# Performance work log

Hardware: AMD Instinct MI355X
Metric: run time of the kernel (lower is better)

Reference implementation:

```python
import jax, jax.numpy as jnp
import numpy as np
from jax.scipy.special import logsumexp

N_STATES = 64
N_OBS = 10000
BATCH = 256
T_MAX = 2048


def setup_inputs() -> dict:
    key = jax.random.key(0)
    k1, k2, k3, k4, k5 = jax.random.split(key, 5)
    x = jax.random.randint(k1, (BATCH, T_MAX), 0, N_OBS, dtype=jnp.int64 if jax.config.jax_enable_x64 else jnp.int32)
    T = jax.random.randint(k2, (BATCH,), 1, T_MAX + 1, dtype=x.dtype)  # lengths in [1, T_MAX]
    pi = jnp.zeros((N_STATES,), dtype=jnp.float32)
    unnormalized_transition_matrix = jax.random.normal(k3, (N_STATES, N_STATES), dtype=jnp.float32)
    unnormalized_emission_matrix = jax.random.normal(k4, (N_STATES, N_OBS), dtype=jnp.float32)
    return {
        "x": x,
        "T": T,
        "pi": pi,
        "unnormalized_transition_matrix": unnormalized_transition_matrix,
        "unnormalized_emission_matrix": unnormalized_emission_matrix,
    }


def reference(x, T, pi, unnormalized_transition_matrix, unnormalized_emission_matrix):
    # log p(x) via the log-domain forward algorithm.
    log_pi = jax.nn.log_softmax(pi, axis=0)                                  # [N]
    log_A = jax.nn.log_softmax(unnormalized_transition_matrix, axis=0)       # [N, N], A[i,k] = p(i | k)-style per torch dim=0
    log_E = jax.nn.log_softmax(unnormalized_emission_matrix, axis=1)         # [N, M]

    # emissions[b, t, n] = log_E[n, x[b, t]]  (gather once, not per step)
    emis = log_E.T[x]                                                        # [B, Tm, N]

    alpha0 = emis[:, 0, :] + log_pi                                          # [B, N]

    def step(alpha, e_t):
        # new_alpha[b, i] = e_t[b, i] + logsumexp_k (log_A[i, k] + alpha[b, k])
        new = e_t + logsumexp(log_A[None, :, :] + alpha[:, None, :], axis=2)
        return new, new

    _, alphas = jax.lax.scan(step, alpha0, jnp.swapaxes(emis[:, 1:, :], 0, 1))  # [Tm-1, B, N]
    log_alpha = jnp.concatenate([alpha0[None], alphas], axis=0)              # [Tm, B, N]

    log_sums = logsumexp(log_alpha, axis=2).T                                # [B, Tm]
    idx = (T - 1).astype(jnp.int32)[:, None]
    log_probs = jnp.take_along_axis(log_sums, idx, axis=1)                   # [B, 1]
    return log_probs
```

## Files before the change

### kernel.cpp

```cpp
#include <hip/hip_runtime.h>
#include <math.h>

#define NS   64
#define NOBS 10000
#define NB   256
#define TMAX 2048

#define PIP_OFF 0
#define ASW_OFF 64
#define LSE_OFF (64 + 4096)
#define ET_OFF  (64 + 4096 + 64)

__device__ __forceinline__ float wsum64(float v) {
  v += __shfl_xor(v, 1);
  v += __shfl_xor(v, 2);
  v += __shfl_xor(v, 4);
  v += __shfl_xor(v, 8);
  v += __shfl_xor(v, 16);
  v += __shfl_xor(v, 32);
  return v;
}

#define DPPROR(S, N)                                                           \
  __int_as_float(__builtin_amdgcn_update_dpp(                                  \
      0, __float_as_int(S), 0x120 + (N), 0xF, 0xF, true))

#define COMB(Q) ({                                                             \
    float a32_ = (Q); float b32_;                                              \
    asm("v_mov_b32 %0, %1" : "=v"(b32_) : "v"(a32_));                          \
    asm("v_permlane32_swap_b32 %0, %1" : "+v"(a32_), "+v"(b32_));              \
    float s32_ = a32_ + b32_;                                                  \
    float a16_ = s32_; float b16_;                                             \
    asm("v_mov_b32 %0, %1" : "=v"(b16_) : "v"(s32_));                          \
    asm("v_permlane16_swap_b32 %0, %1" : "+v"(a16_), "+v"(b16_));              \
    a16_ + b16_; })

__global__ __launch_bounds__(64) void prep_small(const float* __restrict__ pi,
                                                 const float* __restrict__ A,
                                                 float* __restrict__ ws) {
  const int l = threadIdx.x;
  const int r = l & 15, c = l >> 4;
  float p = pi[l];
  float m = p;
  m = fmaxf(m, __shfl_xor(m, 1));
  m = fmaxf(m, __shfl_xor(m, 2));
  m = fmaxf(m, __shfl_xor(m, 4));
  m = fmaxf(m, __shfl_xor(m, 8));
  m = fmaxf(m, __shfl_xor(m, 16));
  m = fmaxf(m, __shfl_xor(m, 32));
  float ex = expf(p - m);
  float s = wsum64(ex);
  ws[PIP_OFF + l] = ex / s;

  __shared__ float Ap[NS * NS];
  float cm = -3.0e38f;
  for (int i = 0; i < NS; ++i) cm = fmaxf(cm, A[i * NS + l]);
  float cs = 0.f;
  for (int i = 0; i < NS; ++i) cs += expf(A[i * NS + l] - cm);
  float inv = 1.0f / cs;
  for (int i = 0; i < NS; ++i) Ap[i * NS + l] = expf(A[i * NS + l] - cm) * inv;
  __syncthreads();

  const int probe = __builtin_amdgcn_update_dpp(0, l, 0x121, 0xF, 0xF, true);
  const int dir = ((probe & 15) == ((r - 1) & 15)) ? 1 : -1;

  for (int g = 0; g < 4; ++g)
    for (int j = 0; j < 16; ++j)
      ws[ASW_OFF + l * 64 + g * 16 + j] =
          Ap[(r + 16 * g) * NS + (16 * c + ((r - dir * j) & 15))];
}

__global__ __launch_bounds__(256) void emis_lse(const float* __restrict__ E,
                                                float* __restrict__ ws) {
  const int s = blockIdx.x;
  const float* row = E + (size_t)s * NOBS;
  __shared__ float red[4];
  float m = -3.0e38f;
  for (int o = threadIdx.x; o < NOBS; o += 256) m = fmaxf(m, row[o]);
  m = fmaxf(m, __shfl_xor(m, 1));
  m = fmaxf(m, __shfl_xor(m, 2));
  m = fmaxf(m, __shfl_xor(m, 4));
  m = fmaxf(m, __shfl_xor(m, 8));
  m = fmaxf(m, __shfl_xor(m, 16));
  m = fmaxf(m, __shfl_xor(m, 32));
  const int wid = threadIdx.x >> 6;
  if ((threadIdx.x & 63) == 0) red[wid] = m;
  __syncthreads();
  m = fmaxf(fmaxf(red[0], red[1]), fmaxf(red[2], red[3]));
  __syncthreads();
  float sum = 0.f;
  for (int o = threadIdx.x; o < NOBS; o += 256) sum += expf(row[o] - m);
  sum = wsum64(sum);
  if ((threadIdx.x & 63) == 0) red[wid] = sum;
  __syncthreads();
  if (threadIdx.x == 0)
    ws[LSE_OFF + s] = m + logf(red[0] + red[1] + red[2] + red[3]);
}

__global__ __launch_bounds__(256) void emis_fill(const float* __restrict__ E,
                                                 float* __restrict__ ws) {
  const int idx = blockIdx.x * 256 + threadIdx.x;
  if (idx >= NS * NOBS) return;
  const int s = idx & 63;
  const int obs = idx >> 6;
  ws[ET_OFF + idx] = expf(E[(size_t)s * NOBS + obs] - ws[LSE_OFF + s]);
}


#define PIN8(i)                                                                \
  asm volatile("" : "+v"(aw[(i)]), "+v"(aw[(i) + 1]), "+v"(aw[(i) + 2]),       \
                    "+v"(aw[(i) + 3]), "+v"(aw[(i) + 4]), "+v"(aw[(i) + 5]),   \
                    "+v"(aw[(i) + 6]), "+v"(aw[(i) + 7]))
#define PIN_AW() do { PIN8(0); PIN8(8); PIN8(16); PIN8(24);                    \
                      PIN8(32); PIN8(40); PIN8(48); PIN8(56); } while (0)

#define STAGE_CHUNK(XS, HALF) do {                                             \
    _Pragma("unroll")                                                          \
    for (int k_ = 0; k_ < 64; ++k_) {                                          \
      const int xt_ = __builtin_amdgcn_readlane((XS), k_);                     \
      const float* gp_ = ET + ((size_t)(unsigned)xt_ << 6) + lane;             \
      __builtin_amdgcn_global_load_lds(gp_, &ebuf[(((HALF) << 6) + k_) << 6],  \
                                       4, 0, 0);                               \
    } } while (0)

#define EREAD(DST, ADDR, IMM)                                                  \
  asm volatile("ds_read_b32 %0, %1 offset:" #IMM : "=v"(DST) : "v"(ADDR))

#define STEP(u, EC) do {                                                       \
    const int t_ = t0 + (u);                                                   \
    const float e_ = EC[(u)];                                                  \
    const unsigned srf_ = __builtin_amdgcn_readfirstlane(__float_as_uint(s));  \
    const int se_ = (int)((srf_ >> 23) & 0xFFu) - 127;                         \
    const float sc_ = __uint_as_float((unsigned)(127 - se_) << 23);            \
    const float es_ = e_ * sc_;                                                \
    float rot[16];                                                             \
    rot[0] = s;                                                                \
    rot[1] = DPPROR(s, 1);   rot[2] = DPPROR(s, 2);   rot[3] = DPPROR(s, 3);   \
    rot[4] = DPPROR(s, 4);   rot[5] = DPPROR(s, 5);   rot[6] = DPPROR(s, 6);   \
    rot[7] = DPPROR(s, 7);   rot[8] = DPPROR(s, 8);   rot[9] = DPPROR(s, 9);   \
    rot[10] = DPPROR(s, 10); rot[11] = DPPROR(s, 11); rot[12] = DPPROR(s, 12); \
    rot[13] = DPPROR(s, 13); rot[14] = DPPROR(s, 14); rot[15] = DPPROR(s, 15); \
    float q0a_ = 0.f, q1a_ = 0.f, q2a_ = 0.f, q3a_ = 0.f;                      \
    float q0b_ = 0.f, q1b_ = 0.f, q2b_ = 0.f, q3b_ = 0.f;                      \
    _Pragma("unroll")                                                          \
    for (int j_ = 0; j_ < 8; ++j_) {                                           \
      q0a_ = fmaf(aw[j_],      rot[j_], q0a_);                                 \
      q1a_ = fmaf(aw[16 + j_], rot[j_], q1a_);                                 \
      q2a_ = fmaf(aw[32 + j_], rot[j_], q2a_);                                 \
      q3a_ = fmaf(aw[48 + j_], rot[j_], q3a_);                                 \
      q0b_ = fmaf(aw[8 + j_],  rot[8 + j_], q0b_);                             \
      q1b_ = fmaf(aw[24 + j_], rot[8 + j_], q1b_);                             \
      q2b_ = fmaf(aw[40 + j_], rot[8 + j_], q2b_);                             \
      q3b_ = fmaf(aw[56 + j_], rot[8 + j_], q3b_);                             \
    }                                                                          \
    const float tot0_ = COMB(q0a_ + q0b_);                                     \
    const float tot1_ = COMB(q1a_ + q1b_);                                     \
    const float tot2_ = COMB(q2a_ + q2b_);                                     \
    const float tot3_ = COMB(q3a_ + q3b_);                                     \
    const float ta_ = (cgrp & 1) ? tot1_ : tot0_;                              \
    const float tb_ = (cgrp & 1) ? tot3_ : tot2_;                              \
    const float sel_ = (cgrp & 2) ? tb_ : ta_;                                 \
    const float w_ = es_ * ((t_ == 0) ? pip : sel_);                           \
    E2 += se_;                                                                 \
    if (t_ == Tn - 1) { vs = w_; e2s = E2; }                                   \
    s = w_;                                                                    \
  } while (0)

#define GROUP(T0, ECUR, ENXT) do {                                             \
    const int t0 = (T0);                                                       \
    { const unsigned ea_ =                                                     \
          ebase + ((unsigned)(((t0 + 4) & 127)) << 8) + ((unsigned)lane << 2); \
      EREAD(ENXT[0], ea_, 0);   EREAD(ENXT[1], ea_, 256);                      \
      EREAD(ENXT[2], ea_, 512); EREAD(ENXT[3], ea_, 768); }                    \
    asm volatile("s_waitcnt lgkmcnt(4)");                                      \
    __builtin_amdgcn_sched_barrier(0);                                         \
    STEP(0, ECUR); STEP(1, ECUR); STEP(2, ECUR); STEP(3, ECUR);                \
  } while (0)

__global__ void __attribute__((amdgpu_flat_work_group_size(64, 64)))
__attribute__((amdgpu_waves_per_eu(1, 1)))
hmm_fwd(const int* __restrict__ x, const int* __restrict__ T,
        const float* __restrict__ ws, float* __restrict__ out) {
  const int lane = threadIdx.x;
  const int b = blockIdx.x;
  const int cgrp = lane >> 4;
  const float* __restrict__ ET = ws + ET_OFF;
  const int* __restrict__ xb = x + (size_t)b * TMAX;
  const int Tn = T[b];

  __shared__ __align__(16) float ebuf[128 * 64];
  const unsigned ebase = (unsigned)(size_t)ebuf;

  float aw[NS];
  {
    const float4* ar = (const float4*)(ws + ASW_OFF + lane * NS);
#pragma unroll
    for (int q = 0; q < 16; ++q) {
      float4 f = ar[q];
      aw[4 * q + 0] = f.x; aw[4 * q + 1] = f.y;
      aw[4 * q + 2] = f.z; aw[4 * q + 3] = f.w;
    }
  }
  PIN_AW();

  const float pip = ws[PIP_OFF + lane];

  int xcur = xb[lane];
  STAGE_CHUNK(xcur, 0);
  int xnext = xb[64 + lane];
  asm volatile("s_waitcnt vmcnt(0)" ::: "memory");

  float eA[4], eB[4];
  {
    const unsigned ea_ = ebase + ((unsigned)lane << 2);
    EREAD(eA[0], ea_, 0);   EREAD(eA[1], ea_, 256);
    EREAD(eA[2], ea_, 512); EREAD(eA[3], ea_, 768);
  }

  float s = 1.0f;
  float vs = 0.f;
  int E2 = 0, e2s = 0;

  const int nch = (Tn + 63) >> 6;
  for (int c = 0; c < nch; ++c) {
    const int tb = c << 6;
    if (c + 1 < TMAX / 64) STAGE_CHUNK(xnext, (c + 1) & 1);
    xnext = ((c + 2) < TMAX / 64) ? xb[((c + 2) << 6) + lane] : 0;
#pragma unroll 1
    for (int gp = 0; gp < 7; ++gp) {
      GROUP(tb + (gp << 3), eA, eB);
      GROUP(tb + (gp << 3) + 4, eB, eA);
    }
    GROUP(tb + 56, eA, eB);
    asm volatile("s_waitcnt vmcnt(0)" ::: "memory");
    GROUP(tb + 60, eB, eA);
  }

  const float sf = wsum64(vs);
  if (lane == 0) {
    const double lp = (double)logf(sf) + (double)e2s * 0.6931471805599453;
    out[b] = (float)lp;
  }
}

extern "C" void kernel_launch(void* const* d_in, const int* in_sizes, int n_in,
                              void* d_out, int out_size, void* d_ws, size_t ws_size,
                              hipStream_t stream) {
  const int*   x  = (const int*)d_in[0];
  const int*   T  = (const int*)d_in[1];
  const float* pi = (const float*)d_in[2];
  const float* A  = (const float*)d_in[3];
  const float* E  = (const float*)d_in[4];
  float* out = (float*)d_out;
  float* ws  = (float*)d_ws;

  prep_small<<<1, 64, 0, stream>>>(pi, A, ws);
  emis_lse<<<NS, 256, 0, stream>>>(E, ws);
  emis_fill<<<(NS * NOBS + 255) / 256, 256, 0, stream>>>(E, ws);
  hmm_fwd<<<NB, 64, 0, stream>>>(x, T, ws, out);
}
```

Before: 462.2 us.

## Use packed FP32 FMA for the transition matvec and rescale every other step

Reorders the swizzled transition matrix so each lane holds pairs of rows (r, r+16) and (r+32, r+48) as float2. The per-step 64-term dot product then runs as v_pk_fma_f32 with the rotated state broadcast, halving the FMA instruction count on the serial critical path. Exponent rescaling via readfirstlane now happens only on odd steps, which removes scalar work but lets values grow over two steps before renormalising. This carries some overflow/underflow risk and relies on inline asm for the packed ops.

Result: slower. 483.2 us (+4.5%).

```diff
diff --git a/kernel.cpp b/kernel.cpp
--- a/kernel.cpp
+++ b/kernel.cpp
@@ -24,6 +24,15 @@
 #define DPPROR(S, N)                                                           \
   __int_as_float(__builtin_amdgcn_update_dpp(                                  \
       0, __float_as_int(S), 0x120 + (N), 0xF, 0xF, true))
+
+#define PKMUL(ACC, AP, RT)                                                     \
+  asm("v_pk_mul_f32 %0, %1, %2 op_sel:[0,0] op_sel_hi:[1,0]"                   \
+      : "=v"(ACC) : "v"(AP), "v"(RT))
+#define PKFMA(ACC, AP, RT)                                                     \
+  asm("v_pk_fma_f32 %0, %1, %2, %3 op_sel:[0,0,0] op_sel_hi:[1,0,1]"           \
+      : "=v"(ACC) : "v"(AP), "v"(RT), "v"(ACC))
+#define PKADD(D, X, Y)                                                         \
+  asm("v_pk_add_f32 %0, %1, %2" : "=v"(D) : "v"(X), "v"(Y))
 
 #define COMB(Q) ({                                                             \
     float a32_ = (Q); float b32_;                                              \
@@ -64,10 +73,13 @@
   const int probe = __builtin_amdgcn_update_dpp(0, l, 0x121, 0xF, 0xF, true);
   const int dir = ((probe & 15) == ((r - 1) & 15)) ? 1 : -1;
 
-  for (int g = 0; g < 4; ++g)
-    for (int j = 0; j < 16; ++j)
-      ws[ASW_OFF + l * 64 + g * 16 + j] =
-          Ap[(r + 16 * g) * NS + (16 * c + ((r - dir * j) & 15))];
+  for (int j = 0; j < 16; ++j) {
+    const int col = 16 * c + ((r - dir * j) & 15);
+    ws[ASW_OFF + l * 64 + 2 * j]          = Ap[(r + 0)  * NS + col];
+    ws[ASW_OFF + l * 64 + 2 * j + 1]      = Ap[(r + 16) * NS + col];
+    ws[ASW_OFF + l * 64 + 32 + 2 * j]     = Ap[(r + 32) * NS + col];
+    ws[ASW_OFF + l * 64 + 32 + 2 * j + 1] = Ap[(r + 48) * NS + col];
+  }
 }
 
 __global__ __launch_bounds__(256) void emis_lse(const float* __restrict__ E,
@@ -107,12 +119,11 @@
 }
 
 
-#define PIN8(i)                                                                \
-  asm volatile("" : "+v"(aw[(i)]), "+v"(aw[(i) + 1]), "+v"(aw[(i) + 2]),       \
-                    "+v"(aw[(i) + 3]), "+v"(aw[(i) + 4]), "+v"(aw[(i) + 5]),   \
-                    "+v"(aw[(i) + 6]), "+v"(aw[(i) + 7]))
-#define PIN_AW() do { PIN8(0); PIN8(8); PIN8(16); PIN8(24);                    \
-                      PIN8(32); PIN8(40); PIN8(48); PIN8(56); } while (0)
+#define PINP(P) asm volatile("" : "+v"((P).x), "+v"((P).y))
+#define PIN_ALL() do {                                                         \
+    _Pragma("unroll")                                                          \
+    for (int q_ = 0; q_ < 16; ++q_) { PINP(a01[q_]); PINP(a23[q_]); }          \
+  } while (0)
 
 #define STAGE_CHUNK(XS, HALF) do {                                             \
     _Pragma("unroll")                                                          \
@@ -129,39 +140,48 @@
 #define STEP(u, EC) do {                                                       \
     const int t_ = t0 + (u);                                                   \
     const float e_ = EC[(u)];                                                  \
-    const unsigned srf_ = __builtin_amdgcn_readfirstlane(__float_as_uint(s));  \
-    const int se_ = (int)((srf_ >> 23) & 0xFFu) - 127;                         \
-    const float sc_ = __uint_as_float((unsigned)(127 - se_) << 23);            \
-    const float es_ = e_ * sc_;                                                \
-    float rot[16];                                                             \
-    rot[0] = s;                                                                \
-    rot[1] = DPPROR(s, 1);   rot[2] = DPPROR(s, 2);   rot[3] = DPPROR(s, 3);   \
-    rot[4] = DPPROR(s, 4);   rot[5] = DPPROR(s, 5);   rot[6] = DPPROR(s, 6);   \
-    rot[7] = DPPROR(s, 7);   rot[8] = DPPROR(s, 8);   rot[9] = DPPROR(s, 9);   \
-    rot[10] = DPPROR(s, 10); rot[11] = DPPROR(s, 11); rot[12] = DPPROR(s, 12); \
-    rot[13] = DPPROR(s, 13); rot[14] = DPPROR(s, 14); rot[15] = DPPROR(s, 15); \
-    float q0a_ = 0.f, q1a_ = 0.f, q2a_ = 0.f, q3a_ = 0.f;                      \
-    float q0b_ = 0.f, q1b_ = 0.f, q2b_ = 0.f, q3b_ = 0.f;                      \
+    float es_;                                                                 \
+    if (((u) & 1) != 0) {               \
+      const unsigned srf_ = __builtin_amdgcn_readfirstlane(__float_as_uint(s));\
+      const int se_ = (int)((srf_ >> 23) & 0xFFu) - 127;                       \
+      const float sc_ = __uint_as_float((unsigned)(127 - se_) << 23);          \
+      es_ = e_ * sc_;                                                          \
+      E2 += se_;                                                               \
+    } else {                                                                   \
+      es_ = e_;                                                                \
+    }                                                                          \
+    rot2[0].x = s;                                                             \
+    rot2[1].x = DPPROR(s, 1);   rot2[2].x = DPPROR(s, 2);                      \
+    rot2[3].x = DPPROR(s, 3);   rot2[4].x = DPPROR(s, 4);                      \
+    rot2[5].x = DPPROR(s, 5);   rot2[6].x = DPPROR(s, 6);                      \
+    rot2[7].x = DPPROR(s, 7);   rot2[8].x = DPPROR(s, 8);                      \
+    rot2[9].x = DPPROR(s, 9);   rot2[10].x = DPPROR(s, 10);                    \
+    rot2[11].x = DPPROR(s, 11); rot2[12].x = DPPROR(s, 12);                    \
+    rot2[13].x = DPPROR(s, 13); rot2[14].x = DPPROR(s, 14);                    \
+    rot2[15].x = DPPROR(s, 15);                                                \
+    float2 ac01a, ac01b, ac23a, ac23b;                                         \
+    PKMUL(ac01a, a01[0], rot2[0]);                                             \
+    PKMUL(ac23a, a23[0], rot2[0]);                                             \
+    PKMUL(ac01b, a01[8], rot2[8]);                                             \
+    PKMUL(ac23b, a23[8], rot2[8]);                                             \
     _Pragma("unroll")                                                          \
-    for (int j_ = 0; j_ < 8; ++j_) {                                           \
-      q0a_ = fmaf(aw[j_],      rot[j_], q0a_);                                 \
-      q1a_ = fmaf(aw[16 + j_], rot[j_], q1a_);                                 \
-      q2a_ = fmaf(aw[32 + j_], rot[j_], q2a_);                                 \
-      q3a_ = fmaf(aw[48 + j_], rot[j_], q3a_);                                 \
-      q0b_ = fmaf(aw[8 + j_],  rot[8 + j_], q0b_);                             \
-      q1b_ = fmaf(aw[24 + j_], rot[8 + j_], q1b_);                             \
-      q2b_ = fmaf(aw[40 + j_], rot[8 + j_], q2b_);                             \
-      q3b_ = fmaf(aw[56 + j_], rot[8 + j_], q3b_);                             \
+    for (int j_ = 1; j_ < 8; ++j_) {                                           \
+      PKFMA(ac01a, a01[j_],     rot2[j_]);                                     \
+      PKFMA(ac23a, a23[j_],     rot2[j_]);                                     \
+      PKFMA(ac01b, a01[8 + j_], rot2[8 + j_]);                                 \
+      PKFMA(ac23b, a23[8 + j_], rot2[8 + j_]);                                 \
     }                                                                          \
-    const float tot0_ = COMB(q0a_ + q0b_);                                     \
-    const float tot1_ = COMB(q1a_ + q1b_);                                     \
-    const float tot2_ = COMB(q2a_ + q2b_);                                     \
-    const float tot3_ = COMB(q3a_ + q3b_);                                     \
+    float2 s01_, s23_;                                                         \
+    PKADD(s01_, ac01a, ac01b);                                                 \
+    PKADD(s23_, ac23a, ac23b);                                                 \
+    const float tot0_ = COMB(s01_.x);                                          \
+    const float tot1_ = COMB(s01_.y);                                          \
+    const float tot2_ = COMB(s23_.x);                                          \
+    const float tot3_ = COMB(s23_.y);                                          \
     const float ta_ = (cgrp & 1) ? tot1_ : tot0_;                              \
     const float tb_ = (cgrp & 1) ? tot3_ : tot2_;                              \
     const float sel_ = (cgrp & 2) ? tb_ : ta_;                                 \
     const float w_ = es_ * ((t_ == 0) ? pip : sel_);                           \
-    E2 += se_;                                                                 \
     if (t_ == Tn - 1) { vs = w_; e2s = E2; }                                   \
     s = w_;                                                                    \
   } while (0)
@@ -191,19 +211,29 @@
   __shared__ __align__(16) float ebuf[128 * 64];
   const unsigned ebase = (unsigned)(size_t)ebuf;
 
-  float aw[NS];
+  float2 a01[16], a23[16];
   {
     const float4* ar = (const float4*)(ws + ASW_OFF + lane * NS);
 #pragma unroll
-    for (int q = 0; q < 16; ++q) {
+    for (int q = 0; q < 8; ++q) {
       float4 f = ar[q];
-      aw[4 * q + 0] = f.x; aw[4 * q + 1] = f.y;
-      aw[4 * q + 2] = f.z; aw[4 * q + 3] = f.w;
+      a01[2 * q]     = make_float2(f.x, f.y);
+      a01[2 * q + 1] = make_float2(f.z, f.w);
     }
-  }
-  PIN_AW();
+#pragma unroll
+    for (int q = 0; q < 8; ++q) {
+      float4 f = ar[8 + q];
+      a23[2 * q]     = make_float2(f.x, f.y);
+      a23[2 * q + 1] = make_float2(f.z, f.w);
+    }
+  }
+  PIN_ALL();
 
   const float pip = ws[PIP_OFF + lane];
+
+  float2 rot2[16];
+#pragma unroll
+  for (int j = 0; j < 16; ++j) rot2[j].y = 0.0f;
 
   int xcur = xb[lane];
   STAGE_CHUNK(xcur, 0);
```

## Fuse DPP rotations into FMAs and use transpose-style cross-row reduction

Applied to the files above, without the earlier changes.

Replaces the separate DPP row-rotate moves plus FMAs with inline-asm v_fmac_f32_dpp instructions that rotate the operand inside the multiply-add. The four per-group partial sums are now combined with a butterfly exchange (two permlane32 swaps, then one permlane16 swap) instead of four full permlane reductions followed by a select. Rescaling by the wavefront's leading exponent now happens only every other step. Together these shorten the serial per-step critical path of the recurrence, at the cost of hand-written DPP hazards (s_nop) and a wider dynamic range between rescales.

New measurement: 456.2 us. No clear change (-1.3%).

```diff
diff --git a/kernel.cpp b/kernel.cpp
--- a/kernel.cpp
+++ b/kernel.cpp
@@ -20,20 +20,6 @@
   v += __shfl_xor(v, 32);
   return v;
 }
-
-#define DPPROR(S, N)                                                           \
-  __int_as_float(__builtin_amdgcn_update_dpp(                                  \
-      0, __float_as_int(S), 0x120 + (N), 0xF, 0xF, true))
-
-#define COMB(Q) ({                                                             \
-    float a32_ = (Q); float b32_;                                              \
-    asm("v_mov_b32 %0, %1" : "=v"(b32_) : "v"(a32_));                          \
-    asm("v_permlane32_swap_b32 %0, %1" : "+v"(a32_), "+v"(b32_));              \
-    float s32_ = a32_ + b32_;                                                  \
-    float a16_ = s32_; float b16_;                                             \
-    asm("v_mov_b32 %0, %1" : "=v"(b16_) : "v"(s32_));                          \
-    asm("v_permlane16_swap_b32 %0, %1" : "+v"(a16_), "+v"(b16_));              \
-    a16_ + b16_; })
 
 __global__ __launch_bounds__(64) void prep_small(const float* __restrict__ pi,
                                                  const float* __restrict__ A,
@@ -126,42 +112,73 @@
 #define EREAD(DST, ADDR, IMM)                                                  \
   asm volatile("ds_read_b32 %0, %1 offset:" #IMM : "=v"(DST) : "v"(ADDR))
 
+#define MVBLK(QA, QB, SV, B, HEAD)                                             \
+  asm volatile(HEAD                                                            \
+    "v_mul_f32 %0, %2, %3\n\t"                                                 \
+    "v_mul_f32_dpp %1, %2, %11 row_ror:8 row_mask:0xf bank_mask:0xf\n\t"       \
+    "v_fmac_f32_dpp %0, %2, %4 row_ror:1 row_mask:0xf bank_mask:0xf\n\t"       \
+    "v_fmac_f32_dpp %1, %2, %12 row_ror:9 row_mask:0xf bank_mask:0xf\n\t"      \
+    "v_fmac_f32_dpp %0, %2, %5 row_ror:2 row_mask:0xf bank_mask:0xf\n\t"       \
+    "v_fmac_f32_dpp %1, %2, %13 row_ror:10 row_mask:0xf bank_mask:0xf\n\t"     \
+    "v_fmac_f32_dpp %0, %2, %6 row_ror:3 row_mask:0xf bank_mask:0xf\n\t"       \
+    "v_fmac_f32_dpp %1, %2, %14 row_ror:11 row_mask:0xf bank_mask:0xf\n\t"     \
+    "v_fmac_f32_dpp %0, %2, %7 row_ror:4 row_mask:0xf bank_mask:0xf\n\t"       \
+    "v_fmac_f32_dpp %1, %2, %15 row_ror:12 row_mask:0xf bank_mask:0xf\n\t"     \
+    "v_fmac_f32_dpp %0, %2, %8 row_ror:5 row_mask:0xf bank_mask:0xf\n\t"       \
+    "v_fmac_f32_dpp %1, %2, %16 row_ror:13 row_mask:0xf bank_mask:0xf\n\t"     \
+    "v_fmac_f32_dpp %0, %2, %9 row_ror:6 row_mask:0xf bank_mask:0xf\n\t"       \
+    "v_fmac_f32_dpp %1, %2, %17 row_ror:14 row_mask:0xf bank_mask:0xf\n\t"     \
+    "v_fmac_f32_dpp %0, %2, %10 row_ror:7 row_mask:0xf bank_mask:0xf\n\t"      \
+    "v_fmac_f32_dpp %1, %2, %18 row_ror:15 row_mask:0xf bank_mask:0xf"         \
+    : "=&v"(QA), "=&v"(QB)                                                     \
+    : "v"(SV),                                                                 \
+      "v"(aw[(B) + 0]), "v"(aw[(B) + 1]), "v"(aw[(B) + 2]), "v"(aw[(B) + 3]),  \
+      "v"(aw[(B) + 4]), "v"(aw[(B) + 5]), "v"(aw[(B) + 6]), "v"(aw[(B) + 7]),  \
+      "v"(aw[(B) + 8]), "v"(aw[(B) + 9]), "v"(aw[(B) + 10]), "v"(aw[(B) + 11]),\
+      "v"(aw[(B) + 12]), "v"(aw[(B) + 13]), "v"(aw[(B) + 14]), "v"(aw[(B) + 15]))
+
 #define STEP(u, EC) do {                                                       \
     const int t_ = t0 + (u);                                                   \
     const float e_ = EC[(u)];                                                  \
-    const unsigned srf_ = __builtin_amdgcn_readfirstlane(__float_as_uint(s));  \
-    const int se_ = (int)((srf_ >> 23) & 0xFFu) - 127;                         \
-    const float sc_ = __uint_as_float((unsigned)(127 - se_) << 23);            \
-    const float es_ = e_ * sc_;                                                \
-    float rot[16];                                                             \
-    rot[0] = s;                                                                \
-    rot[1] = DPPROR(s, 1);   rot[2] = DPPROR(s, 2);   rot[3] = DPPROR(s, 3);   \
-    rot[4] = DPPROR(s, 4);   rot[5] = DPPROR(s, 5);   rot[6] = DPPROR(s, 6);   \
-    rot[7] = DPPROR(s, 7);   rot[8] = DPPROR(s, 8);   rot[9] = DPPROR(s, 9);   \
-    rot[10] = DPPROR(s, 10); rot[11] = DPPROR(s, 11); rot[12] = DPPROR(s, 12); \
-    rot[13] = DPPROR(s, 13); rot[14] = DPPROR(s, 14); rot[15] = DPPROR(s, 15); \
-    float q0a_ = 0.f, q1a_ = 0.f, q2a_ = 0.f, q3a_ = 0.f;                      \
-    float q0b_ = 0.f, q1b_ = 0.f, q2b_ = 0.f, q3b_ = 0.f;                      \
-    _Pragma("unroll")                                                          \
-    for (int j_ = 0; j_ < 8; ++j_) {                                           \
-      q0a_ = fmaf(aw[j_],      rot[j_], q0a_);                                 \
-      q1a_ = fmaf(aw[16 + j_], rot[j_], q1a_);                                 \
-      q2a_ = fmaf(aw[32 + j_], rot[j_], q2a_);                                 \
-      q3a_ = fmaf(aw[48 + j_], rot[j_], q3a_);                                 \
-      q0b_ = fmaf(aw[8 + j_],  rot[8 + j_], q0b_);                             \
-      q1b_ = fmaf(aw[24 + j_], rot[8 + j_], q1b_);                             \
-      q2b_ = fmaf(aw[40 + j_], rot[8 + j_], q2b_);                             \
-      q3b_ = fmaf(aw[56 + j_], rot[8 + j_], q3b_);                             \
-    }                                                                          \
-    const float tot0_ = COMB(q0a_ + q0b_);                                     \
-    const float tot1_ = COMB(q1a_ + q1b_);                                     \
-    const float tot2_ = COMB(q2a_ + q2b_);                                     \
-    const float tot3_ = COMB(q3a_ + q3b_);                                     \
-    const float ta_ = (cgrp & 1) ? tot1_ : tot0_;                              \
-    const float tb_ = (cgrp & 1) ? tot3_ : tot2_;                              \
-    const float sel_ = (cgrp & 2) ? tb_ : ta_;                                 \
-    const float w_ = es_ * ((t_ == 0) ? pip : sel_);                           \
-    E2 += se_;                                                                 \
+    float es_;                                                                 \
+    if (((u) & 1) != 0) {               \
+      const unsigned srf_ = __builtin_amdgcn_readfirstlane(__float_as_uint(s));\
+      const int se_ = (int)((srf_ >> 23) & 0xFFu) - 127;                       \
+      es_ = e_ * __uint_as_float((unsigned)(127 - se_) << 23);                 \
+      E2 += se_;                                                               \
+    } else { es_ = e_; }                                                       \
+    float qa0_, qb0_, qa1_, qb1_, qa2_, qb2_, qa3_, qb3_;                      \
+    MVBLK(qa0_, qb0_, s, 0,  "s_nop 1\n\t");                                   \
+    MVBLK(qa1_, qb1_, s, 16, "");                                              \
+    MVBLK(qa2_, qb2_, s, 32, "");                                              \
+    MVBLK(qa3_, qb3_, s, 48, "");                                              \
+    const float q0_ = qa0_ + qb0_;                                             \
+    const float q1_ = qa1_ + qb1_;                                             \
+    const float q2_ = qa2_ + qb2_;                                             \
+    const float q3_ = qa3_ + qb3_;                                             \
+    \
+    float em_ = c1m ? q0_ : q2_;              \
+    float en_ = c1m ? q1_ : q3_;              \
+    float emc_, enc_;                                                          \
+    asm("v_mov_b32 %0, %1" : "=v"(emc_) : "v"(em_));                           \
+    asm("v_mov_b32 %0, %1" : "=v"(enc_) : "v"(en_));                           \
+    asm("v_permlane32_swap_b32 %0, %1" : "+v"(em_), "+v"(emc_));               \
+    asm("v_permlane32_swap_b32 %0, %1" : "+v"(en_), "+v"(enc_));               \
+    const float pm_ = lo32 ? em_ : emc_;                 \
+    const float pn_ = lo32 ? en_ : enc_;                 \
+    const float ka_ = c1m ? q2_ : q0_;                  \
+    const float kb_ = c1m ? q3_ : q1_;                  \
+    const float ua_ = ka_ + pm_;                                               \
+    const float ub_ = kb_ + pn_;                                               \
+                                           \
+    float gv_ = c0m ? ua_ : ub_;                     \
+    float gvc_;                                                                \
+    asm("v_mov_b32 %0, %1" : "=v"(gvc_) : "v"(gv_));                           \
+    asm("v_permlane16_swap_b32 %0, %1" : "+v"(gv_), "+v"(gvc_));               \
+    const float pg_ = lo16 ? gv_ : gvc_;                                       \
+    const float kp_ = c0m ? ub_ : ua_;                                         \
+    const float fin_ = kp_ + pg_;                                              \
+    const float w_ = es_ * ((t_ == 0) ? pip : fin_);                           \
     if (t_ == Tn - 1) { vs = w_; e2s = E2; }                                   \
     s = w_;                                                                    \
   } while (0)
@@ -184,6 +201,10 @@
   const int lane = threadIdx.x;
   const int b = blockIdx.x;
   const int cgrp = lane >> 4;
+  const bool c0m = (cgrp & 1) != 0;
+  const bool c1m = (cgrp & 2) != 0;
+  const bool lo32 = lane < 32;
+  const bool lo16 = (lane & 16) == 0;
   const float* __restrict__ ET = ws + ET_OFF;
   const int* __restrict__ xb = x + (size_t)b * TMAX;
   const int Tn = T[b];
```
